# Performance work log

Measured on AMD Instinct MI355X. Metric: run time of the kernel, lower is better.

The kernel has to match this reference:

```python
import jax, jax.numpy as jnp
import numpy as np

GS = 14           # group_size = (14, 14); N must equal GS*GS
NUM_HEADS = 4
DIM = 128
POS_DIM = (DIM // 4) // 4  # 8
EPS = 1e-5


def _ln(x, g, b):
    mu = x.mean(-1, keepdims=True)
    var = ((x - mu) ** 2).mean(-1, keepdims=True)
    return (x - mu) * jax.lax.rsqrt(var + EPS) * g + b


def setup_inputs() -> dict:
    key = jax.random.key(0)
    ks = jax.random.split(key, 20)
    B, N, C = 1024, GS * GS, DIM
    s = lambda fan: 1.0 / np.sqrt(fan)
    inp = {
        "x": jax.random.normal(ks[0], (B, N, C), jnp.float32),
        # linear weights stored as [in, out] (torch W.T)
        "wq": jax.random.normal(ks[1], (C, C), jnp.float32) * s(C),
        "wkv": jax.random.normal(ks[2], (C, 2 * C), jnp.float32) * s(C),
        "wproj": jax.random.normal(ks[3], (C, C), jnp.float32) * s(C),
        "bproj": jnp.zeros((C,), jnp.float32),
        "pp_w": jax.random.normal(ks[4], (2, POS_DIM), jnp.float32) * s(2),
        "pp_b": jnp.zeros((POS_DIM,), jnp.float32),
        "ln1_g": jnp.ones((POS_DIM,), jnp.float32),
        "ln1_b": jnp.zeros((POS_DIM,), jnp.float32),
        "l1_w": jax.random.normal(ks[5], (POS_DIM, POS_DIM), jnp.float32) * s(POS_DIM),
        "l1_b": jnp.zeros((POS_DIM,), jnp.float32),
        "ln2_g": jnp.ones((POS_DIM,), jnp.float32),
        "ln2_b": jnp.zeros((POS_DIM,), jnp.float32),
        "l2_w": jax.random.normal(ks[6], (POS_DIM, POS_DIM), jnp.float32) * s(POS_DIM),
        "l2_b": jnp.zeros((POS_DIM,), jnp.float32),
        "ln3_g": jnp.ones((POS_DIM,), jnp.float32),
        "ln3_b": jnp.zeros((POS_DIM,), jnp.float32),
        "l3_w": jax.random.normal(ks[7], (POS_DIM, NUM_HEADS), jnp.float32) * s(POS_DIM),
        "l3_b": jnp.zeros((NUM_HEADS,), jnp.float32),
    }
    return inp


def _rel_pos_index():
    # relative_position_index for square window (len(group_size)==2 branch)
    ch = jnp.arange(GS)
    coords = jnp.stack(jnp.meshgrid(ch, ch, indexing="ij"))        # [2, GS, GS]
    cf = coords.reshape(2, -1)                                       # [2, N]
    rel = cf[:, :, None] - cf[:, None, :]                            # [2, N, N]
    rel = rel.transpose(1, 2, 0)                                     # [N, N, 2]
    rel = rel + jnp.array([GS - 1, GS - 1])
    idx = rel[..., 0] * (2 * GS - 1) + rel[..., 1]                   # [N, N]
    return idx


def _biases():
    p = jnp.arange(1 - GS, GS)
    b = jnp.stack(jnp.meshgrid(p, p, indexing="ij"))                 # [2, 2GS-1, 2GS-1]
    return b.reshape(2, -1).T.astype(jnp.float32)                    # [(2GS-1)^2, 2]


def reference(x, wq, wkv, wproj, bproj, pp_w, pp_b,
              ln1_g, ln1_b, l1_w, l1_b,
              ln2_g, ln2_b, l2_w, l2_b,
              ln3_g, ln3_b, l3_w, l3_b):
    B, N, C = x.shape
    H = NUM_HEADS
    hd = C // H
    scale = hd ** -0.5

    q = (x @ wq).reshape(B, N, H, hd).transpose(0, 2, 1, 3)          # [B,H,N,hd]
    kv = (x @ wkv).reshape(B, N, 2, H, hd)
    k = kv[:, :, 0].transpose(0, 2, 1, 3)                            # [B,H,N,hd]
    v = kv[:, :, 1].transpose(0, 2, 1, 3)

    attn = jnp.einsum("bhqd,bhkd->bhqk", q, k) * scale               # [B,H,N,N]

    # dynamic position bias: tiny MLP over relative coords, residual=False path
    pos = _biases() @ pp_w + pp_b                                    # [M, pos_dim]
    pos = jax.nn.relu(_ln(pos, ln1_g, ln1_b)) @ l1_w + l1_b
    pos = jax.nn.relu(_ln(pos, ln2_g, ln2_b)) @ l2_w + l2_b
    pos = jax.nn.relu(_ln(pos, ln3_g, ln3_b)) @ l3_w + l3_b          # [M, H]

    rpb = pos[_rel_pos_index()]                                      # [N,N,H] gather
    attn = attn + rpb.transpose(2, 0, 1)[None]                       # [B,H,N,N]

    attn = jax.nn.softmax(attn, axis=-1)
    out = jnp.einsum("bhqk,bhkd->bhqd", attn, v)                     # [B,H,N,hd]
    out = out.transpose(0, 2, 1, 3).reshape(B, N, C)
    return out @ wproj + bproj
```

## Files before the change

kernel.cpp:

```cpp
#include <hip/hip_runtime.h>

typedef __attribute__((ext_vector_type(8))) __bf16 bf16x8;
typedef __attribute__((ext_vector_type(4))) __bf16 bf16x4;
typedef __attribute__((ext_vector_type(4))) float f32x4;
typedef __attribute__((ext_vector_type(4))) short s16x4;
typedef __attribute__((ext_vector_type(8))) short s16x8;

#define MFMA32(a,b,c) __builtin_amdgcn_mfma_f32_16x16x32_bf16(a, b, c, 0, 0, 0)

static __device__ inline f32x4 MFMAX16(s16x4 a, s16x4 b, f32x4 c) {
#if __has_builtin(__builtin_amdgcn_mfma_f32_16x16x16bf16_1k)
  return __builtin_amdgcn_mfma_f32_16x16x16bf16_1k(a, b, c, 0, 0, 0);
#else
  f32x4 d;
  asm("v_mfma_f32_16x16x16_bf16 %0, %1, %2, %3" : "=v"(d) : "v"(a), "v"(b), "v"(c));
  return d;
#endif
}

#define KS 40
#define VS 212
#define NW 4
#define LOG2E 1.4426950408889634f

__device__ inline void lnrelu8(float* v, const float* g, const float* bta) {
  float mu = 0.f;
#pragma unroll
  for (int i = 0; i < 8; i++) mu += v[i];
  mu *= 0.125f;
  float var = 0.f;
#pragma unroll
  for (int i = 0; i < 8; i++) { float d = v[i] - mu; var += d * d; }
  var *= 0.125f;
  float inv = rsqrtf(var + 1e-5f);
#pragma unroll
  for (int i = 0; i < 8; i++) v[i] = fmaxf((v[i] - mu) * inv * g[i] + bta[i], 0.f);
}

__global__ void k_prep(const float* __restrict__ wq, const float* __restrict__ wkv,
                       const float* __restrict__ wproj,
                       const float* __restrict__ pp_w, const float* __restrict__ pp_b,
                       const float* ln1_g, const float* ln1_b, const float* l1_w, const float* l1_b,
                       const float* ln2_g, const float* ln2_b, const float* l2_w, const float* l2_b,
                       const float* ln3_g, const float* ln3_b, const float* l3_w, const float* l3_b,
                       __bf16* __restrict__ wF, __bf16* __restrict__ wpT,
                       __bf16* __restrict__ biasP) {
  __shared__ float pos_s[4 * 729];
  int blk = blockIdx.x, tid = threadIdx.x;
  if (blk < 88) {
    int t = blk * 256 + tid;
    if (t < 6144) {
      int lane = t & 63, frag = t >> 6;
      int kc = frag & 3, nt = (frag >> 2) & 1, tt = (frag >> 3) % 3, h = frag / 24;
      int col = lane & 15, quad = lane >> 4;
      int o = h * 32 + nt * 16 + col;
      int ibase = kc * 32 + quad * 8;
      bf16x8 vv;
#pragma unroll
      for (int j = 0; j < 8; j++) {
        int in = ibase + j;
        float w = (tt == 0) ? wq[in * 128 + o]
                : (tt == 1) ? wkv[in * 256 + o]
                            : wkv[in * 256 + 128 + o];
        vv[j] = (__bf16)w;
      }
      *(bf16x8*)&wF[(size_t)t * 8] = vv;
    } else if (t < 6144 + 16384) {
      int t2 = t - 6144;
      int o = t2 >> 7, i = t2 & 127;
      wpT[t2] = (__bf16)wproj[i * 128 + o];
    }
    return;
  }
  for (int m = tid; m < 729; m += 256) {
    float dr = (float)(m / 27) - 13.f, dc = (float)(m % 27) - 13.f;
    float a[8], bv[8];
#pragma unroll
    for (int j = 0; j < 8; j++) a[j] = dr * pp_w[j] + dc * pp_w[8 + j] + pp_b[j];
    lnrelu8(a, ln1_g, ln1_b);
#pragma unroll
    for (int o = 0; o < 8; o++) {
      float s = l1_b[o];
#pragma unroll
      for (int j = 0; j < 8; j++) s += a[j] * l1_w[j * 8 + o];
      bv[o] = s;
    }
    lnrelu8(bv, ln2_g, ln2_b);
#pragma unroll
    for (int o = 0; o < 8; o++) {
      float s = l2_b[o];
#pragma unroll
      for (int j = 0; j < 8; j++) s += bv[j] * l2_w[j * 8 + o];
      a[o] = s;
    }
    lnrelu8(a, ln3_g, ln3_b);
#pragma unroll
    for (int o = 0; o < 4; o++) {
      float s = l3_b[o];
#pragma unroll
      for (int j = 0; j < 8; j++) s += a[j] * l3_w[j * 4 + o];
      pos_s[o * 729 + m] = s;
    }
  }
  __syncthreads();
  int t = (blk - 88) * 256 + tid;
  int g = t % 52; int rem = t / 52; int qi = rem % 208; int h = rem / 208;
  int kt = g >> 2, qd = g & 3;
  int kj0 = g * 4;
  int r1 = qi / 14, c1 = qi % 14;
  bf16x4 o;
#pragma unroll
  for (int r = 0; r < 4; r++) {
    int kj = kj0 + r;
    float v = 0.f;
    if (qi < 196 && kj < 196) {
      int r2 = kj / 14, c2 = kj % 14;
      v = pos_s[h * 729 + (r1 - r2 + 13) * 27 + (c1 - c2 + 13)];
    }
    o[r] = (__bf16)(v * LOG2E);
  }
  *(bf16x4*)&biasP[(((size_t)h * 208 + qi) * 4 + qd) * 52 + kt * 4] = o;
}

__launch_bounds__(256, 4)
__global__ void k_attn(const float* __restrict__ x, const __bf16* __restrict__ wF,
                       const __bf16* __restrict__ biasP, __bf16* __restrict__ Og) {
  __shared__ __align__(16) __bf16 k_s[208 * KS];
  __shared__ __align__(16) __bf16 vT_s[32 * VS];

  int tid = threadIdx.x;
  int wv = tid >> 6, lane = tid & 63, col = lane & 15, quad = lane >> 4;
  int bi = blockIdx.x;
  int b = (bi & 7) * 128 + (bi >> 5);
  int h = (bi >> 3) & 3;

  const __bf16* wH = wF + (size_t)h * 12288;
#define WG(t, nt, kc) (*(const bf16x8*)&wH[(((t) * 2 + (nt)) * 4 + (kc)) * 512 + lane * 8])

  const float* xb = x + (size_t)b * (196 * 128);
  const float scale = 0.17677669529663687f * LOG2E;

  s16x4 qb[4][2];
  float4 xr[8];

  {
    int row0 = wv * 16 + col;
    const float4* q4 = (const float4*)(xb + (size_t)(row0 < 196 ? row0 : 0) * 128 + quad * 8);
#pragma unroll
    for (int kc = 0; kc < 4; kc++) { xr[2 * kc] = q4[kc * 8]; xr[2 * kc + 1] = q4[kc * 8 + 1]; }
  }

#pragma unroll
  for (int i = 0; i < 4; i++) {
    int qt = wv + i * NW;
    if (qt < 13) {
      bf16x8 xf[4];
#pragma unroll
      for (int kc = 0; kc < 4; kc++) {
        float4 u = xr[2 * kc], v = xr[2 * kc + 1];
        bf16x8 r;
        r[0] = (__bf16)u.x; r[1] = (__bf16)u.y; r[2] = (__bf16)u.z; r[3] = (__bf16)u.w;
        r[4] = (__bf16)v.x; r[5] = (__bf16)v.y; r[6] = (__bf16)v.z; r[7] = (__bf16)v.w;
        xf[kc] = r;
      }
      int qn = qt + NW;
      if (i < 3 && qn < 13) {
        int row = qn * 16 + col;
        const float4* q4 = (const float4*)(xb + (size_t)(row < 196 ? row : 0) * 128 + quad * 8);
#pragma unroll
        for (int kc = 0; kc < 4; kc++) { xr[2 * kc] = q4[kc * 8]; xr[2 * kc + 1] = q4[kc * 8 + 1]; }
      }
      int row = qt * 16 + col;
#pragma unroll
      for (int nt = 0; nt < 2; nt++) {
        f32x4 acc = {0.f, 0.f, 0.f, 0.f};
#pragma unroll
        for (int kc = 0; kc < 4; kc++) acc = MFMA32(WG(1, nt, kc), xf[kc], acc);
        bf16x4 pk;
#pragma unroll
        for (int r = 0; r < 4; r++) pk[r] = (__bf16)acc[r];
        *(bf16x4*)&k_s[row * KS + quad * 8 + nt * 4] = pk;
      }
#pragma unroll
      for (int nt = 0; nt < 2; nt++) {
        f32x4 acc = {0.f, 0.f, 0.f, 0.f};
#pragma unroll
        for (int kc = 0; kc < 4; kc++) acc = MFMA32(xf[kc], WG(2, nt, kc), acc);
        bf16x4 pk;
#pragma unroll
        for (int r = 0; r < 4; r++) pk[r] = (__bf16)acc[r];
        *(bf16x4*)&vT_s[(nt * 16 + col) * VS + qt * 16 + quad * 4] = pk;
      }
#pragma unroll
      for (int nt = 0; nt < 2; nt++) {
        f32x4 acc = {0.f, 0.f, 0.f, 0.f};
#pragma unroll
        for (int kc = 0; kc < 4; kc++) acc = MFMA32(WG(0, nt, kc), xf[kc], acc);
        bf16x4 pk;
#pragma unroll
        for (int r = 0; r < 4; r++) pk[r] = (__bf16)(acc[r] * scale);
        qb[i][nt] = __builtin_bit_cast(s16x4, pk);
      }
    }
  }

  bf16x4 bl[13];
  {
    int qi0 = wv * 16 + col;
    const __bf16* bp = biasP + (((size_t)h * 208 + qi0) * 4 + quad) * 52;
#pragma unroll
    for (int kt = 0; kt < 13; kt++) bl[kt] = *(const bf16x4*)(bp + kt * 4);
  }
  __syncthreads();

#pragma unroll
  for (int i = 0; i < 4; i++) {
    int qt = wv + i * NW;
    if (qt < 13) {
      int qi = qt * 16 + col;
      int qn = qt + NW;
      bool nxt = (i < 3) && (qn < 13);
      const __bf16* bpn = biasP + (((size_t)h * 208 + (qn * 16 + col)) * 4 + quad) * 52;

      float sum = 0.f;
      f32x4 o0a = {0.f,0.f,0.f,0.f}, o0b = {0.f,0.f,0.f,0.f};
      f32x4 o1a = {0.f,0.f,0.f,0.f}, o1b = {0.f,0.f,0.f,0.f};
#pragma unroll
      for (int kt = 0; kt < 13; kt++) {
        s16x8 ka = *(const s16x8*)&k_s[(kt * 16 + col) * KS + quad * 8];
        s16x4 ka0 = __builtin_shufflevector(ka, ka, 0, 1, 2, 3);
        s16x4 ka1 = __builtin_shufflevector(ka, ka, 4, 5, 6, 7);
        f32x4 acc = {0.f, 0.f, 0.f, 0.f};
        acc = MFMAX16(ka0, qb[i][0], acc);
        acc = MFMAX16(ka1, qb[i][1], acc);
        bf16x4 b4 = bl[kt];
        if (nxt) bl[kt] = *(const bf16x4*)(bpn + kt * 4);
        bf16x4 pk;
#pragma unroll
        for (int r = 0; r < 4; r++) {
          float e = __builtin_amdgcn_exp2f(acc[r] + (float)b4[r]);
          if (kt == 12 && quad != 0) e = 0.f;
          sum += e;
          pk[r] = (__bf16)e;
        }
        s16x4 pv = __builtin_bit_cast(s16x4, pk);
        s16x4 va0 = *(const s16x4*)&vT_s[col * VS + kt * 16 + quad * 4];
        s16x4 va1 = *(const s16x4*)&vT_s[(16 + col) * VS + kt * 16 + quad * 4];
        if (kt & 1) { o0b = MFMAX16(va0, pv, o0b); o1b = MFMAX16(va1, pv, o1b); }
        else        { o0a = MFMAX16(va0, pv, o0a); o1a = MFMAX16(va1, pv, o1a); }
      }
      sum += __shfl_xor(sum, 16);
      sum += __shfl_xor(sum, 32);
      float inv = 1.f / sum;
      if (qi < 196) {
        __bf16* og = Og + ((size_t)b * 196 + qi) * 128 + h * 32;
        bf16x4 s0, s1;
#pragma unroll
        for (int r = 0; r < 4; r++) {
          s0[r] = (__bf16)((o0a[r] + o0b[r]) * inv);
          s1[r] = (__bf16)((o1a[r] + o1b[r]) * inv);
        }
        *(bf16x4*)&og[quad * 4]      = s0;
        *(bf16x4*)&og[16 + quad * 4] = s1;
      }
    }
  }
#undef WG
}

__launch_bounds__(256, 4)
__global__ void k_proj(const __bf16* __restrict__ Og, const __bf16* __restrict__ wpT,
                       const float* __restrict__ bproj, float* __restrict__ out) {
  int tid = threadIdx.x, wv = tid >> 6, lane = tid & 63, col = lane & 15, quad = lane >> 4;
  size_t rb = (size_t)blockIdx.x * 64 + wv * 16;
  const __bf16* arow = Og + (rb + col) * 128 + quad * 8;
  bf16x8 af[4];
#pragma unroll
  for (int kc = 0; kc < 4; kc++) af[kc] = *(const bf16x8*)(arow + kc * 32);
#pragma unroll
  for (int nt = 0; nt < 8; nt++) {
    f32x4 acc = {0.f, 0.f, 0.f, 0.f};
#pragma unroll
    for (int kc = 0; kc < 4; kc++)
      acc = MFMA32(*(const bf16x8*)&wpT[(size_t)(nt * 16 + col) * 128 + kc * 32 + quad * 8],
                   af[kc], acc);
    int od = nt * 16 + quad * 4;
    float4 bp = *(const float4*)&bproj[od];
    float4 st = { acc[0] + bp.x, acc[1] + bp.y, acc[2] + bp.z, acc[3] + bp.w };
    *(float4*)&out[(rb + col) * 128 + od] = st;
  }
}

extern "C" void kernel_launch(void* const* d_in, const int* in_sizes, int n_in,
                              void* d_out, int out_size, void* d_ws, size_t ws_size,
                              hipStream_t stream) {
  const float* x     = (const float*)d_in[0];
  const float* wq    = (const float*)d_in[1];
  const float* wkv   = (const float*)d_in[2];
  const float* wproj = (const float*)d_in[3];
  const float* bproj = (const float*)d_in[4];
  const float* pp_w  = (const float*)d_in[5];
  const float* pp_b  = (const float*)d_in[6];
  const float* ln1_g = (const float*)d_in[7];
  const float* ln1_b = (const float*)d_in[8];
  const float* l1_w  = (const float*)d_in[9];
  const float* l1_b  = (const float*)d_in[10];
  const float* ln2_g = (const float*)d_in[11];
  const float* ln2_b = (const float*)d_in[12];
  const float* l2_w  = (const float*)d_in[13];
  const float* l2_b  = (const float*)d_in[14];
  const float* ln3_g = (const float*)d_in[15];
  const float* ln3_b = (const float*)d_in[16];
  const float* l3_w  = (const float*)d_in[17];
  const float* l3_b  = (const float*)d_in[18];
  float* out = (float*)d_out;

  char* ws = (char*)d_ws;
  __bf16* wF    = (__bf16*)ws;
  __bf16* wpT   = (__bf16*)(ws + 98304);
  __bf16* biasP = (__bf16*)(ws + 131072);
  __bf16* Og    = (__bf16*)(ws + 477184);

  k_prep<<<257, 256, 0, stream>>>(wq, wkv, wproj, pp_w, pp_b,
                                  ln1_g, ln1_b, l1_w, l1_b,
                                  ln2_g, ln2_b, l2_w, l2_b,
                                  ln3_g, ln3_b, l3_w, l3_b,
                                  wF, wpT, biasP);
  k_attn<<<4096, 256, 0, stream>>>(x, wF, biasP, Og);
  k_proj<<<3136, 256, 0, stream>>>(Og, wpT, bproj, out);
}
```

Measured before the change: 415.5 us.

## Fuse attention and output projection, one block per batch with K/V in registers

Restructures the attention kernel so each block handles one batch element with one wave per head. K and V are held entirely in registers instead of shared memory, and the per-head outputs are staged in shared memory. The output projection then runs in the same kernel, which removes the separate projection launch and the bf16 intermediate round-trip through global memory. In exchange, register pressure rises sharply (K and V for 13 tiles per lane), the grid drops to 1024 blocks with less parallelism, and x is read three times per wave.

```diff
diff --git a/kernel.cpp b/kernel.cpp
--- a/kernel.cpp
+++ b/kernel.cpp
@@ -4,7 +4,6 @@
 typedef __attribute__((ext_vector_type(4))) __bf16 bf16x4;
 typedef __attribute__((ext_vector_type(4))) float f32x4;
 typedef __attribute__((ext_vector_type(4))) short s16x4;
-typedef __attribute__((ext_vector_type(8))) short s16x8;
 
 #define MFMA32(a,b,c) __builtin_amdgcn_mfma_f32_16x16x32_bf16(a, b, c, 0, 0, 0)
 
@@ -18,10 +17,8 @@
 #endif
 }
 
-#define KS 40
-#define VS 212
-#define NW 4
 #define LOG2E 1.4426950408889634f
+#define OS 136
 
 __device__ inline void lnrelu8(float* v, const float* g, const float* bta) {
   float mu = 0.f;
@@ -122,173 +119,198 @@
   *(bf16x4*)&biasP[(((size_t)h * 208 + qi) * 4 + qd) * 52 + kt * 4] = o;
 }
 
-__launch_bounds__(256, 4)
+__launch_bounds__(256)
 __global__ void k_attn(const float* __restrict__ x, const __bf16* __restrict__ wF,
-                       const __bf16* __restrict__ biasP, __bf16* __restrict__ Og) {
-  __shared__ __align__(16) __bf16 k_s[208 * KS];
-  __shared__ __align__(16) __bf16 vT_s[32 * VS];
-
-  int tid = threadIdx.x;
-  int wv = tid >> 6, lane = tid & 63, col = lane & 15, quad = lane >> 4;
-  int bi = blockIdx.x;
-  int b = (bi & 7) * 128 + (bi >> 5);
-  int h = (bi >> 3) & 3;
-
+                       const __bf16* __restrict__ biasP, const __bf16* __restrict__ wpT,
+                       const float* __restrict__ bproj, float* __restrict__ out) {
+  __shared__ __align__(16) __bf16 O_s[196 * OS];
+
+  const int tid = threadIdx.x;
+  const int h = tid >> 6, lane = tid & 63, col = lane & 15, quad = lane >> 4;
+  const int b = blockIdx.x;
   const __bf16* wH = wF + (size_t)h * 12288;
 #define WG(t, nt, kc) (*(const bf16x8*)&wH[(((t) * 2 + (nt)) * 4 + (kc)) * 512 + lane * 8])
-
   const float* xb = x + (size_t)b * (196 * 128);
   const float scale = 0.17677669529663687f * LOG2E;
 
-  s16x4 qb[4][2];
-  float4 xr[8];
+#define LOADX(buf, t) do { \
+    int row_ = (t) * 16 + col; \
+    const float4* q4_ = (const float4*)(xb + (size_t)(row_ < 196 ? row_ : 0) * 128 + quad * 8); \
+    _Pragma("unroll") \
+    for (int kc_ = 0; kc_ < 4; kc_++) { buf[2*kc_] = q4_[kc_*8]; buf[2*kc_+1] = q4_[kc_*8+1]; } \
+  } while (0)
+
+#define CVTX(xf, buf) do { \
+    _Pragma("unroll") \
+    for (int kc_ = 0; kc_ < 4; kc_++) { \
+      float4 u_ = buf[2*kc_], v_ = buf[2*kc_+1]; \
+      bf16x8 r_; \
+      r_[0]=(__bf16)u_.x; r_[1]=(__bf16)u_.y; r_[2]=(__bf16)u_.z; r_[3]=(__bf16)u_.w; \
+      r_[4]=(__bf16)v_.x; r_[5]=(__bf16)v_.y; r_[6]=(__bf16)v_.z; r_[7]=(__bf16)v_.w; \
+      xf[kc_] = r_; \
+    } \
+  } while (0)
+
+  s16x4 kreg[13][2];
+  s16x4 vreg[13][2];
 
   {
-    int row0 = wv * 16 + col;
-    const float4* q4 = (const float4*)(xb + (size_t)(row0 < 196 ? row0 : 0) * 128 + quad * 8);
-#pragma unroll
-    for (int kc = 0; kc < 4; kc++) { xr[2 * kc] = q4[kc * 8]; xr[2 * kc + 1] = q4[kc * 8 + 1]; }
-  }
-
-#pragma unroll
-  for (int i = 0; i < 4; i++) {
-    int qt = wv + i * NW;
-    if (qt < 13) {
+    bf16x8 kw[8];
+#pragma unroll
+    for (int nt = 0; nt < 2; nt++)
+#pragma unroll
+      for (int kc = 0; kc < 4; kc++) kw[nt * 4 + kc] = WG(1, nt, kc);
+    float4 x0[8], x1[8];
+    LOADX(x0, 0); LOADX(x1, 1);
+#pragma unroll
+    for (int kt = 0; kt < 13; kt++) {
       bf16x8 xf[4];
-#pragma unroll
-      for (int kc = 0; kc < 4; kc++) {
-        float4 u = xr[2 * kc], v = xr[2 * kc + 1];
-        bf16x8 r;
-        r[0] = (__bf16)u.x; r[1] = (__bf16)u.y; r[2] = (__bf16)u.z; r[3] = (__bf16)u.w;
-        r[4] = (__bf16)v.x; r[5] = (__bf16)v.y; r[6] = (__bf16)v.z; r[7] = (__bf16)v.w;
-        xf[kc] = r;
-      }
-      int qn = qt + NW;
-      if (i < 3 && qn < 13) {
-        int row = qn * 16 + col;
-        const float4* q4 = (const float4*)(xb + (size_t)(row < 196 ? row : 0) * 128 + quad * 8);
-#pragma unroll
-        for (int kc = 0; kc < 4; kc++) { xr[2 * kc] = q4[kc * 8]; xr[2 * kc + 1] = q4[kc * 8 + 1]; }
-      }
-      int row = qt * 16 + col;
+      if (kt & 1) { CVTX(xf, x1); if (kt + 2 < 13) LOADX(x1, kt + 2); }
+      else        { CVTX(xf, x0); if (kt + 2 < 13) LOADX(x0, kt + 2); }
 #pragma unroll
       for (int nt = 0; nt < 2; nt++) {
         f32x4 acc = {0.f, 0.f, 0.f, 0.f};
 #pragma unroll
-        for (int kc = 0; kc < 4; kc++) acc = MFMA32(WG(1, nt, kc), xf[kc], acc);
+        for (int kc = 0; kc < 4; kc++) acc = MFMA32(kw[nt * 4 + kc], xf[kc], acc);
         bf16x4 pk;
 #pragma unroll
         for (int r = 0; r < 4; r++) pk[r] = (__bf16)acc[r];
-        *(bf16x4*)&k_s[row * KS + quad * 8 + nt * 4] = pk;
-      }
+        kreg[kt][nt] = __builtin_bit_cast(s16x4, pk);
+      }
+    }
+  }
+
+  {
+    bf16x8 vw[8];
+#pragma unroll
+    for (int nt = 0; nt < 2; nt++)
+#pragma unroll
+      for (int kc = 0; kc < 4; kc++) vw[nt * 4 + kc] = WG(2, nt, kc);
+    float4 xv[8];
+    LOADX(xv, 0);
+#pragma unroll
+    for (int kt = 0; kt < 13; kt++) {
+      bf16x8 xf[4];
+      CVTX(xf, xv);
+      if (kt + 1 < 13) LOADX(xv, kt + 1);
 #pragma unroll
       for (int nt = 0; nt < 2; nt++) {
         f32x4 acc = {0.f, 0.f, 0.f, 0.f};
 #pragma unroll
-        for (int kc = 0; kc < 4; kc++) acc = MFMA32(xf[kc], WG(2, nt, kc), acc);
+        for (int kc = 0; kc < 4; kc++) acc = MFMA32(xf[kc], vw[nt * 4 + kc], acc);
         bf16x4 pk;
 #pragma unroll
         for (int r = 0; r < 4; r++) pk[r] = (__bf16)acc[r];
-        *(bf16x4*)&vT_s[(nt * 16 + col) * VS + qt * 16 + quad * 4] = pk;
-      }
-#pragma unroll
-      for (int nt = 0; nt < 2; nt++) {
-        f32x4 acc = {0.f, 0.f, 0.f, 0.f};
-#pragma unroll
-        for (int kc = 0; kc < 4; kc++) acc = MFMA32(WG(0, nt, kc), xf[kc], acc);
+        vreg[kt][nt] = __builtin_bit_cast(s16x4, pk);
+      }
+    }
+  }
+
+  {
+    bf16x8 qw[8];
+#pragma unroll
+    for (int nt = 0; nt < 2; nt++)
+#pragma unroll
+      for (int kc = 0; kc < 4; kc++) qw[nt * 4 + kc] = WG(0, nt, kc);
+    float4 xq[8];
+    LOADX(xq, 0);
+#pragma unroll 1
+    for (int qt = 0; qt < 13; qt++) {
+      bf16x8 xf[4];
+      CVTX(xf, xq);
+      if (qt + 1 < 13) LOADX(xq, qt + 1);
+      s16x4 qb0, qb1;
+      {
+        f32x4 acc = {0.f, 0.f, 0.f, 0.f};
+#pragma unroll
+        for (int kc = 0; kc < 4; kc++) acc = MFMA32(qw[kc], xf[kc], acc);
         bf16x4 pk;
 #pragma unroll
         for (int r = 0; r < 4; r++) pk[r] = (__bf16)(acc[r] * scale);
-        qb[i][nt] = __builtin_bit_cast(s16x4, pk);
-      }
-    }
-  }
-
-  bf16x4 bl[13];
-  {
-    int qi0 = wv * 16 + col;
-    const __bf16* bp = biasP + (((size_t)h * 208 + qi0) * 4 + quad) * 52;
-#pragma unroll
-    for (int kt = 0; kt < 13; kt++) bl[kt] = *(const bf16x4*)(bp + kt * 4);
-  }
-  __syncthreads();
-
-#pragma unroll
-  for (int i = 0; i < 4; i++) {
-    int qt = wv + i * NW;
-    if (qt < 13) {
+        qb0 = __builtin_bit_cast(s16x4, pk);
+      }
+      {
+        f32x4 acc = {0.f, 0.f, 0.f, 0.f};
+#pragma unroll
+        for (int kc = 0; kc < 4; kc++) acc = MFMA32(qw[4 + kc], xf[kc], acc);
+        bf16x4 pk;
+#pragma unroll
+        for (int r = 0; r < 4; r++) pk[r] = (__bf16)(acc[r] * scale);
+        qb1 = __builtin_bit_cast(s16x4, pk);
+      }
       int qi = qt * 16 + col;
-      int qn = qt + NW;
-      bool nxt = (i < 3) && (qn < 13);
-      const __bf16* bpn = biasP + (((size_t)h * 208 + (qn * 16 + col)) * 4 + quad) * 52;
-
-      float sum = 0.f;
+      const __bf16* bp = biasP + (((size_t)h * 208 + qi) * 4 + quad) * 52;
+      f32x4 sums = {0.f, 0.f, 0.f, 0.f};
       f32x4 o0a = {0.f,0.f,0.f,0.f}, o0b = {0.f,0.f,0.f,0.f};
       f32x4 o1a = {0.f,0.f,0.f,0.f}, o1b = {0.f,0.f,0.f,0.f};
 #pragma unroll
       for (int kt = 0; kt < 13; kt++) {
-        s16x8 ka = *(const s16x8*)&k_s[(kt * 16 + col) * KS + quad * 8];
-        s16x4 ka0 = __builtin_shufflevector(ka, ka, 0, 1, 2, 3);
-        s16x4 ka1 = __builtin_shufflevector(ka, ka, 4, 5, 6, 7);
-        f32x4 acc = {0.f, 0.f, 0.f, 0.f};
-        acc = MFMAX16(ka0, qb[i][0], acc);
-        acc = MFMAX16(ka1, qb[i][1], acc);
-        bf16x4 b4 = bl[kt];
-        if (nxt) bl[kt] = *(const bf16x4*)(bpn + kt * 4);
+        bf16x4 bl = *(const bf16x4*)(bp + kt * 4);
+        f32x4 acc = {0.f, 0.f, 0.f, 0.f};
+        acc = MFMAX16(kreg[kt][0], qb0, acc);
+        acc = MFMAX16(kreg[kt][1], qb1, acc);
         bf16x4 pk;
 #pragma unroll
         for (int r = 0; r < 4; r++) {
-          float e = __builtin_amdgcn_exp2f(acc[r] + (float)b4[r]);
+          float e = __builtin_amdgcn_exp2f(acc[r] + (float)bl[r]);
           if (kt == 12 && quad != 0) e = 0.f;
-          sum += e;
+          sums[r] += e;
           pk[r] = (__bf16)e;
         }
         s16x4 pv = __builtin_bit_cast(s16x4, pk);
-        s16x4 va0 = *(const s16x4*)&vT_s[col * VS + kt * 16 + quad * 4];
-        s16x4 va1 = *(const s16x4*)&vT_s[(16 + col) * VS + kt * 16 + quad * 4];
-        if (kt & 1) { o0b = MFMAX16(va0, pv, o0b); o1b = MFMAX16(va1, pv, o1b); }
-        else        { o0a = MFMAX16(va0, pv, o0a); o1a = MFMAX16(va1, pv, o1a); }
-      }
+        if (kt & 1) { o0b = MFMAX16(vreg[kt][0], pv, o0b); o1b = MFMAX16(vreg[kt][1], pv, o1b); }
+        else        { o0a = MFMAX16(vreg[kt][0], pv, o0a); o1a = MFMAX16(vreg[kt][1], pv, o1a); }
+      }
+      float sum = sums[0] + sums[1] + sums[2] + sums[3];
       sum += __shfl_xor(sum, 16);
       sum += __shfl_xor(sum, 32);
       float inv = 1.f / sum;
       if (qi < 196) {
-        __bf16* og = Og + ((size_t)b * 196 + qi) * 128 + h * 32;
+        __bf16* oo = &O_s[qi * OS + h * 32];
         bf16x4 s0, s1;
 #pragma unroll
         for (int r = 0; r < 4; r++) {
           s0[r] = (__bf16)((o0a[r] + o0b[r]) * inv);
           s1[r] = (__bf16)((o1a[r] + o1b[r]) * inv);
         }
-        *(bf16x4*)&og[quad * 4]      = s0;
-        *(bf16x4*)&og[16 + quad * 4] = s1;
+        *(bf16x4*)&oo[quad * 4]      = s0;
+        *(bf16x4*)&oo[16 + quad * 4] = s1;
+      }
+    }
+  }
+  __syncthreads();
+
+  {
+    int t0 = (13 * h) >> 2, t1 = (13 * (h + 1)) >> 2;
+#pragma unroll 1
+    for (int pt = t0; pt < t1; pt++) {
+      int orow = pt * 16 + col;
+      int ar = orow < 196 ? orow : 0;
+      bf16x8 af[4];
+#pragma unroll
+      for (int kc = 0; kc < 4; kc++)
+        af[kc] = *(const bf16x8*)&O_s[ar * OS + kc * 32 + quad * 8];
+      bool valid = orow < 196;
+      float* op = out + ((size_t)b * 196 + orow) * 128;
+#pragma unroll
+      for (int nt = 0; nt < 8; nt++) {
+        f32x4 acc = {0.f, 0.f, 0.f, 0.f};
+#pragma unroll
+        for (int kc = 0; kc < 4; kc++)
+          acc = MFMA32(*(const bf16x8*)&wpT[(size_t)(nt * 16 + col) * 128 + kc * 32 + quad * 8],
+                       af[kc], acc);
+        int od = nt * 16 + quad * 4;
+        float4 bp4 = *(const float4*)&bproj[od];
+        if (valid) {
+          float4 st = { acc[0] + bp4.x, acc[1] + bp4.y, acc[2] + bp4.z, acc[3] + bp4.w };
+          *(float4*)&op[od] = st;
+        }
       }
     }
   }
 #undef WG
-}
-
-__launch_bounds__(256, 4)
-__global__ void k_proj(const __bf16* __restrict__ Og, const __bf16* __restrict__ wpT,
-                       const float* __restrict__ bproj, float* __restrict__ out) {
-  int tid = threadIdx.x, wv = tid >> 6, lane = tid & 63, col = lane & 15, quad = lane >> 4;
-  size_t rb = (size_t)blockIdx.x * 64 + wv * 16;
-  const __bf16* arow = Og + (rb + col) * 128 + quad * 8;
-  bf16x8 af[4];
-#pragma unroll
-  for (int kc = 0; kc < 4; kc++) af[kc] = *(const bf16x8*)(arow + kc * 32);
-#pragma unroll
-  for (int nt = 0; nt < 8; nt++) {
-    f32x4 acc = {0.f, 0.f, 0.f, 0.f};
-#pragma unroll
-    for (int kc = 0; kc < 4; kc++)
-      acc = MFMA32(*(const bf16x8*)&wpT[(size_t)(nt * 16 + col) * 128 + kc * 32 + quad * 8],
-                   af[kc], acc);
-    int od = nt * 16 + quad * 4;
-    float4 bp = *(const float4*)&bproj[od];
-    float4 st = { acc[0] + bp.x, acc[1] + bp.y, acc[2] + bp.z, acc[3] + bp.w };
-    *(float4*)&out[(rb + col) * 128 + od] = st;
-  }
+#undef LOADX
+#undef CVTX
 }
 
 extern "C" void kernel_launch(void* const* d_in, const int* in_sizes, int n_in,
@@ -319,13 +341,11 @@
   __bf16* wF    = (__bf16*)ws;
   __bf16* wpT   = (__bf16*)(ws + 98304);
   __bf16* biasP = (__bf16*)(ws + 131072);
-  __bf16* Og    = (__bf16*)(ws + 477184);
 
   k_prep<<<257, 256, 0, stream>>>(wq, wkv, wproj, pp_w, pp_b,
                                   ln1_g, ln1_b, l1_w, l1_b,
                                   ln2_g, ln2_b, l2_w, l2_b,
                                   ln3_g, ln3_b, l3_w, l3_b,
                                   wF, wpT, biasP);
-  k_attn<<<4096, 256, 0, stream>>>(x, wF, biasP, Og);
-  k_proj<<<3136, 256, 0, stream>>>(Og, wpT, bproj, out);
-}
+  k_attn<<<1024, 256, 0, stream>>>(x, wF, biasP, wpT, bproj, out);
+}
```

Measured after the change: 415.1 us. No clear change (-0.1%).
